# Performance work log

Hardware: AMD Instinct MI355X
Metric: run time of the kernel (lower is better)

Reference implementation:

```python
import jax, jax.numpy as jnp
import numpy as np

B, S, D, H = 4, 2048, 2048, 16
HD = D // H  # 128


def setup_inputs() -> dict:
    key = jax.random.key(0)
    k1, k2, k3 = jax.random.split(key, 3)
    sc = 1.0 / np.sqrt(D)
    return {
        "x": jax.random.normal(k1, (B, S, D), dtype=jnp.float32),
        "W_qkv": jax.random.normal(k2, (D, 3 * D), dtype=jnp.float32) * sc,
        "W_out": jax.random.normal(k3, (D, D), dtype=jnp.float32) * sc,
        "b_out": jnp.zeros((D,), dtype=jnp.float32),
    }


def _rotate_half(t):
    t1, t2 = jnp.split(t, 2, axis=-1)
    return jnp.concatenate([-t2, t1], axis=-1)


def reference(x, W_qkv, W_out, b_out):
    b, s, d = x.shape
    qkv = jnp.einsum('bsd,de->bse', x, W_qkv)  # fused QKV projection
    q, k, v = jnp.split(qkv, 3, axis=-1)
    # [b, h, s, hd]
    q = q.reshape(b, s, H, HD).transpose(0, 2, 1, 3)
    k = k.reshape(b, s, H, HD).transpose(0, 2, 1, 3)
    v = v.reshape(b, s, H, HD).transpose(0, 2, 1, 3)
    # RoPE (NeoX-style half-split), past_kv=None so positions = arange(s)
    pos = jnp.arange(s, dtype=jnp.float32)
    theta = 1.0 / (10000.0 ** (jnp.arange(0, HD, 2, dtype=jnp.float32) / HD))
    angles = pos[:, None] * theta[None, :]           # [s, hd/2]
    cos = jnp.concatenate([jnp.cos(angles)] * 2, -1)  # [s, hd] (repeat halves)
    sin = jnp.concatenate([jnp.sin(angles)] * 2, -1)
    cos = cos[None, None]  # [1,1,s,hd]
    sin = sin[None, None]
    q = q * cos + _rotate_half(q) * sin
    k = k * cos + _rotate_half(k) * sin
    # causal SDPA, scale = 1/sqrt(head_dim)
    scale = 1.0 / jnp.sqrt(jnp.asarray(HD, dtype=q.dtype))
    scores = jnp.einsum('bhqd,bhkd->bhqk', q, k) * scale
    causal = jnp.tril(jnp.ones((s, s), dtype=bool))
    scores = jnp.where(causal[None, None], scores, jnp.finfo(scores.dtype).min)
    attn = jax.nn.softmax(scores, axis=-1)
    out = jnp.einsum('bhqk,bhkd->bhqd', attn, v)
    out = out.transpose(0, 2, 1, 3).reshape(b, s, D)
    return jnp.einsum('bsd,de->bse', out, W_out) + b_out
```

## Files before the change

### kernel.cpp

```cpp
#include <hip/hip_runtime.h>

typedef unsigned short ushort_t;
typedef unsigned int u32;
typedef __attribute__((ext_vector_type(8))) short bf16x8;
typedef __attribute__((ext_vector_type(4))) float f32x4;

#define B_ 4
#define S_ 2048
#define D_ 2048
#define H_ 16
#define HD_ 128

__device__ __forceinline__ ushort_t f2bf(float f) {
  u32 x = __builtin_bit_cast(u32, f);
  x += 0x7fffu + ((x >> 16) & 1u);
  return (ushort_t)(x >> 16);
}
__device__ __forceinline__ float bf2f(ushort_t u) {
  u32 x = ((u32)u) << 16;
  return __builtin_bit_cast(float, x);
}

struct __align__(8) us4 { ushort_t x, y, z, w; };

__global__ void k_cvt_bf16(const float* __restrict__ in, ushort_t* __restrict__ out, int n) {
  int i = (blockIdx.x * 256 + threadIdx.x) * 4;
  if (i >= n) return;
  float4 v = *(const float4*)(in + i);
  us4 o;
  o.x = f2bf(v.x); o.y = f2bf(v.y); o.z = f2bf(v.z); o.w = f2bf(v.w);
  *(us4*)(out + i) = o;
}

__global__ void k_transpose_bf16(const float* __restrict__ in, ushort_t* __restrict__ out,
                                 int R, int C) {
  __shared__ float ld[32][33];
  int c0 = blockIdx.x * 32, r0 = blockIdx.y * 32;
  int tc = threadIdx.x & 31, tr = threadIdx.x >> 5;
#pragma unroll
  for (int i = 0; i < 4; ++i) {
    int r = tr + i * 8;
    ld[r][tc] = in[(size_t)(r0 + r) * C + c0 + tc];
  }
  __syncthreads();
#pragma unroll
  for (int i = 0; i < 4; ++i) {
    int r = tr + i * 8;
    out[(size_t)(c0 + r) * R + r0 + tc] = f2bf(ld[tc][r]);
  }
}

__global__ void k_rope_tables(float* __restrict__ cost, float* __restrict__ sint) {
  int i = blockIdx.x * 256 + threadIdx.x;
  int s = i >> 6, j = i & 63;
  double th = pow(10000.0, -(double)j / 64.0);
  double a = (double)s * th;
  cost[i] = (float)cos(a);
  sint[i] = (float)sin(a);
}

template <int FINAL>
__global__ __launch_bounds__(256, 2) void k_gemm_bt(const ushort_t* __restrict__ A,
                                                    const ushort_t* __restrict__ Bt,
                                                    void* __restrict__ Cout,
                                                    const float* __restrict__ bias,
                                                    int M, int N, int K) {
  __shared__ __attribute__((aligned(16))) ushort_t As[128 * 32];
  __shared__ __attribute__((aligned(16))) ushort_t Bs[128 * 32];
  const int tid = threadIdx.x;
  const int w = tid >> 6, l = tid & 63;
  const int lr = l & 15, lg = l >> 4;
  const int m0 = blockIdx.y * 128, n0 = blockIdx.x * 128;
  const int wr = (w >> 1) * 64, wc = (w & 1) * 64;
  f32x4 acc[4][4] = {};
  for (int kt = 0; kt < K; kt += 32) {
#pragma unroll
    for (int i = 0; i < 2; ++i) {
      int c = i * 256 + w * 64 + l;
      const ushort_t* ga = A + (size_t)(m0 + (c >> 2)) * K + kt + (c & 3) * 8;
      const ushort_t* gb = Bt + (size_t)(n0 + (c >> 2)) * K + kt + (c & 3) * 8;
      __builtin_amdgcn_global_load_lds(
          (const __attribute__((address_space(1))) u32*)ga,
          (__attribute__((address_space(3))) u32*)(As + (size_t)(i * 256 + w * 64) * 8), 16, 0, 0);
      __builtin_amdgcn_global_load_lds(
          (const __attribute__((address_space(1))) u32*)gb,
          (__attribute__((address_space(3))) u32*)(Bs + (size_t)(i * 256 + w * 64) * 8), 16, 0, 0);
    }
    __syncthreads();
    bf16x8 af[4], bfr[4];
#pragma unroll
    for (int m = 0; m < 4; ++m)
      af[m] = *(const bf16x8*)(As + (wr + m * 16 + lr) * 32 + lg * 8);
#pragma unroll
    for (int n = 0; n < 4; ++n)
      bfr[n] = *(const bf16x8*)(Bs + (wc + n * 16 + lr) * 32 + lg * 8);
#pragma unroll
    for (int m = 0; m < 4; ++m)
#pragma unroll
      for (int n = 0; n < 4; ++n)
        acc[m][n] = __builtin_amdgcn_mfma_f32_16x16x32_bf16(af[m], bfr[n], acc[m][n], 0, 0, 0);
    __syncthreads();
  }
#pragma unroll
  for (int m = 0; m < 4; ++m) {
#pragma unroll
    for (int n = 0; n < 4; ++n) {
#pragma unroll
      for (int j = 0; j < 4; ++j) {
        int row = m0 + wr + m * 16 + lg * 4 + j;
        int col = n0 + wc + n * 16 + lr;
        if (FINAL) {
          ((float*)Cout)[(size_t)row * N + col] = acc[m][n][j] + bias[col];
        } else {
          ((ushort_t*)Cout)[(size_t)row * N + col] = f2bf(acc[m][n][j]);
        }
      }
    }
  }
}

__global__ void k_split_rope(const ushort_t* __restrict__ tmp, ushort_t* __restrict__ dst,
                             const float* __restrict__ cost, const float* __restrict__ sint,
                             int mode) {
  int s0 = blockIdx.x * 32;
  int h = blockIdx.y;
  int b = blockIdx.z;
  int bh = b * H_ + h;
  if (mode < 2) {
#pragma unroll
    for (int i = 0; i < 16; ++i) {
      int e = i * 256 + threadIdx.x;
      int sr = e >> 7, d = e & 127;
      int s = s0 + sr;
      size_t base = (size_t)(b * S_ + s) * D_ + h * HD_;
      float v = bf2f(tmp[base + d]);
      int j = d & 63;
      float cth = cost[s * 64 + j], sth = sint[s * 64 + j];
      int pd = (d < 64) ? d + 64 : d - 64;
      float v2 = bf2f(tmp[base + pd]);
      float r = (d < 64) ? v * cth - v2 * sth : v * cth + v2 * sth;
      dst[((size_t)bh * S_ + s) * HD_ + d] = f2bf(r);
    }
  } else {
    __shared__ ushort_t ld[32][132];
#pragma unroll
    for (int i = 0; i < 16; ++i) {
      int e = i * 256 + threadIdx.x;
      int sr = e >> 7, d = e & 127;
      ld[sr][d] = tmp[(size_t)(b * S_ + s0 + sr) * D_ + h * HD_ + d];
    }
    __syncthreads();
#pragma unroll
    for (int i = 0; i < 16; ++i) {
      int e = i * 256 + threadIdx.x;
      int d = e >> 5, sr = e & 31;
      dst[((size_t)bh * HD_ + d) * S_ + s0 + sr] = ld[sr][d];
    }
  }
}

__global__ __launch_bounds__(256, 2) void k_attn2(const ushort_t* __restrict__ Q,
                                                  const ushort_t* __restrict__ K,
                                                  const ushort_t* __restrict__ Vt,
                                                  ushort_t* __restrict__ O) {
  __shared__ __attribute__((aligned(16))) ushort_t Ks[64 * 128];
  __shared__ __attribute__((aligned(16))) ushort_t Vs[128 * 64];
  __shared__ __attribute__((aligned(16))) ushort_t Pl[8][16 * 72];

  int id = blockIdx.x;
  int work = (id & 7) * 128 + (id >> 3);
  int bh = work >> 4;
  int qt = 15 - (work & 15);
  int b = bh >> 4, h = bh & 15;

  const int tid = threadIdx.x;
  const int w = tid >> 6, l = tid & 63;
  const int lr = l & 15, lg = l >> 4;
  const int qb = qt * 128 + w * 32;

  const ushort_t* Qp = Q + (size_t)bh * S_ * HD_;
  const char* Kpb = (const char*)(K + (size_t)bh * S_ * HD_);
  const char* Vpb = (const char*)(Vt + (size_t)bh * HD_ * S_);
  const float scale = 0.08838834764831845f;

  int krow[4], koff[4], vrow[4], voff[4];
#pragma unroll
  for (int r = 0; r < 4; ++r) {
    int c = r * 256 + tid;
    krow[r] = c >> 4;
    koff[r] = (((c & 15) ^ (krow[r] & 7)) << 4);
    vrow[r] = c >> 3;
    voff[r] = (((c & 7) ^ (vrow[r] & 7)) << 4);
  }
  const int swz = (lr & 7) << 4;

  bf16x8 qf[2][4];
#pragma unroll
  for (int f = 0; f < 2; ++f)
#pragma unroll
    for (int dw = 0; dw < 4; ++dw)
      qf[f][dw] = *(const bf16x8*)(Qp + (size_t)(qb + f * 16 + lr) * HD_ + dw * 32 + lg * 8);

  f32x4 oacc[2][8] = {};
  float mr[2] = {-1e30f, -1e30f};
  float lsum[2] = {0.f, 0.f};
  const int nkt = 2 * qt + 2;

  for (int kt = 0; kt < nkt; ++kt) {
    const int kb = kt * 64;
#pragma unroll
    for (int r = 0; r < 4; ++r) {
      __builtin_amdgcn_global_load_lds(
          (const __attribute__((address_space(1))) u32*)(Kpb + (size_t)(kb + krow[r]) * 256 + koff[r]),
          (__attribute__((address_space(3))) u32*)(Ks + (r * 256 + w * 64) * 8), 16, 0, 0);
    }
#pragma unroll
    for (int r = 0; r < 4; ++r) {
      __builtin_amdgcn_global_load_lds(
          (const __attribute__((address_space(1))) u32*)(Vpb + (size_t)vrow[r] * (S_ * 2) + kb * 2 + voff[r]),
          (__attribute__((address_space(3))) u32*)(Vs + (r * 256 + w * 64) * 8), 16, 0, 0);
    }
    __syncthreads();

    if (kb <= qb + 31) {
      f32x4 st[2][4];
      __builtin_amdgcn_s_setprio(1);
#pragma unroll
      for (int t = 0; t < 4; ++t) {
        bf16x8 kf[4];
#pragma unroll
        for (int dw = 0; dw < 4; ++dw)
          kf[dw] = *(const bf16x8*)((const char*)Ks + (t * 16 + lr) * 256 + ((dw * 64 + lg * 16) ^ swz));
        f32x4 a0 = {}, a1 = {};
#pragma unroll
        for (int dw = 0; dw < 4; ++dw) {
          a0 = __builtin_amdgcn_mfma_f32_16x16x32_bf16(kf[dw], qf[0][dw], a0, 0, 0, 0);
          a1 = __builtin_amdgcn_mfma_f32_16x16x32_bf16(kf[dw], qf[1][dw], a1, 0, 0, 0);
        }
        st[0][t] = a0;
        st[1][t] = a1;
      }
      __builtin_amdgcn_s_setprio(0);

#pragma unroll
      for (int f = 0; f < 2; ++f) {
        const int qg = qb + f * 16 + lr;
        float tmax = -1e30f;
#pragma unroll
        for (int t = 0; t < 4; ++t) {
#pragma unroll
          for (int j = 0; j < 4; ++j) {
            int kg = kb + t * 16 + lg * 4 + j;
            float s = st[f][t][j] * scale;
            s = (kg > qg) ? -1e30f : s;
            st[f][t][j] = s;
            tmax = fmaxf(tmax, s);
          }
        }
        tmax = fmaxf(tmax, __shfl_xor(tmax, 16, 64));
        tmax = fmaxf(tmax, __shfl_xor(tmax, 32, 64));
        float mnew = fmaxf(mr[f], tmax);
        float alpha = __expf(mr[f] - mnew);
        mr[f] = mnew;
        float psum = 0.f;
        ushort_t* Pw = Pl[w * 2 + f];
#pragma unroll
        for (int t = 0; t < 4; ++t) {
          float p0 = __expf(st[f][t][0] - mnew);
          float p1 = __expf(st[f][t][1] - mnew);
          float p2 = __expf(st[f][t][2] - mnew);
          float p3 = __expf(st[f][t][3] - mnew);
          psum += (p0 + p1) + (p2 + p3);
          *(u32*)&Pw[lr * 72 + t * 16 + lg * 4] = (u32)f2bf(p0) | ((u32)f2bf(p1) << 16);
          *(u32*)&Pw[lr * 72 + t * 16 + lg * 4 + 2] = (u32)f2bf(p2) | ((u32)f2bf(p3) << 16);
        }
        psum += __shfl_xor(psum, 16, 64);
        psum += __shfl_xor(psum, 32, 64);
        lsum[f] = lsum[f] * alpha + psum;
        float a0 = __shfl(alpha, lg * 4 + 0, 64);
        float a1 = __shfl(alpha, lg * 4 + 1, 64);
        float a2 = __shfl(alpha, lg * 4 + 2, 64);
        float a3 = __shfl(alpha, lg * 4 + 3, 64);
#pragma unroll
        for (int dt = 0; dt < 8; ++dt) {
          oacc[f][dt][0] *= a0;
          oacc[f][dt][1] *= a1;
          oacc[f][dt][2] *= a2;
          oacc[f][dt][3] *= a3;
        }
      }

      __builtin_amdgcn_s_setprio(1);
#pragma unroll
      for (int kw = 0; kw < 2; ++kw) {
        bf16x8 pa0 = *(const bf16x8*)&Pl[w * 2 + 0][lr * 72 + kw * 32 + lg * 8];
        bf16x8 pa1 = *(const bf16x8*)&Pl[w * 2 + 1][lr * 72 + kw * 32 + lg * 8];
#pragma unroll
        for (int dt = 0; dt < 8; ++dt) {
          bf16x8 vf = *(const bf16x8*)((const char*)Vs + (dt * 16 + lr) * 128 + ((kw * 64 + lg * 16) ^ swz));
          oacc[0][dt] = __builtin_amdgcn_mfma_f32_16x16x32_bf16(pa0, vf, oacc[0][dt], 0, 0, 0);
          oacc[1][dt] = __builtin_amdgcn_mfma_f32_16x16x32_bf16(pa1, vf, oacc[1][dt], 0, 0, 0);
        }
      }
      __builtin_amdgcn_s_setprio(0);
    }
    __syncthreads();
  }

#pragma unroll
  for (int f = 0; f < 2; ++f) {
    float l0 = __shfl(lsum[f], lg * 4 + 0, 64);
    float l1 = __shfl(lsum[f], lg * 4 + 1, 64);
    float l2 = __shfl(lsum[f], lg * 4 + 2, 64);
    float l3 = __shfl(lsum[f], lg * 4 + 3, 64);
    float i0 = 1.f / l0, i1 = 1.f / l1, i2 = 1.f / l2, i3 = 1.f / l3;
    ushort_t* Op = O + (size_t)(b * S_ + qb + f * 16) * D_ + h * HD_;
#pragma unroll
    for (int dt = 0; dt < 8; ++dt) {
      Op[(size_t)(lg * 4 + 0) * D_ + dt * 16 + lr] = f2bf(oacc[f][dt][0] * i0);
      Op[(size_t)(lg * 4 + 1) * D_ + dt * 16 + lr] = f2bf(oacc[f][dt][1] * i1);
      Op[(size_t)(lg * 4 + 2) * D_ + dt * 16 + lr] = f2bf(oacc[f][dt][2] * i2);
      Op[(size_t)(lg * 4 + 3) * D_ + dt * 16 + lr] = f2bf(oacc[f][dt][3] * i3);
    }
  }
}

extern "C" void kernel_launch(void* const* d_in, const int* in_sizes, int n_in,
                              void* d_out, int out_size, void* d_ws, size_t ws_size,
                              hipStream_t stream) {
  const float* x = (const float*)d_in[0];
  const float* Wqkv = (const float*)d_in[1];
  const float* Wout = (const float*)d_in[2];
  const float* bout = (const float*)d_in[3];
  char* ws = (char*)d_ws;

  ushort_t* xb = (ushort_t*)(ws + 0);
  ushort_t* Wqt = (ushort_t*)(ws + 33554432ull);
  ushort_t* tmp = (ushort_t*)(ws + 58720256ull);
  ushort_t* Qb = (ushort_t*)(ws + 92274688ull);
  ushort_t* Kb = (ushort_t*)(ws + 125829120ull);
  ushort_t* Vb = (ushort_t*)(ws + 159383552ull);
  float* cost = (float*)(ws + 192937984ull);
  float* sint = (float*)(ws + 193462272ull);

  const int M = B_ * S_;

  k_cvt_bf16<<<dim3((M * D_) / 4 / 256), 256, 0, stream>>>(x, xb, M * D_);
  k_transpose_bf16<<<dim3(3 * D_ / 32, D_ / 32), 256, 0, stream>>>(Wqkv, Wqt, D_, 3 * D_);
  k_rope_tables<<<dim3(S_ * 64 / 256), 256, 0, stream>>>(cost, sint);

  for (int p = 0; p < 3; ++p) {
    k_gemm_bt<0><<<dim3(D_ / 128, M / 128), 256, 0, stream>>>(
        xb, Wqt + (size_t)p * D_ * D_, tmp, nullptr, M, D_, D_);
    ushort_t* dst = (p == 0) ? Qb : (p == 1) ? Kb : Vb;
    k_split_rope<<<dim3(S_ / 32, H_, B_), 256, 0, stream>>>(tmp, dst, cost, sint, p);
  }

  k_attn2<<<dim3((S_ / 128) * B_ * H_), 256, 0, stream>>>(Qb, Kb, Vb, xb );

  k_transpose_bf16<<<dim3(D_ / 32, D_ / 32), 256, 0, stream>>>(Wout, tmp, D_, D_);
  k_gemm_bt<1><<<dim3(D_ / 128, M / 128), 256, 0, stream>>>(
      xb, tmp, d_out, bout, M, D_, D_);
}
```

Before: 590.6 us.

## Rewrite GEMM and attention with larger tiles and multi-buffered async loads

```diff
diff --git a/kernel.cpp b/kernel.cpp
--- a/kernel.cpp
+++ b/kernel.cpp
@@ -20,6 +20,11 @@
   u32 x = ((u32)u) << 16;
   return __builtin_bit_cast(float, x);
 }
+
+#define GLL16(srcp, ldsp)                                            \
+  __builtin_amdgcn_global_load_lds(                                  \
+      (const __attribute__((address_space(1))) u32*)(srcp),          \
+      (__attribute__((address_space(3))) u32*)(ldsp), 16, 0, 0)
 
 struct __align__(8) us4 { ushort_t x, y, z, w; };
 
@@ -60,63 +65,126 @@
 }
 
 template <int FINAL>
-__global__ __launch_bounds__(256, 2) void k_gemm_bt(const ushort_t* __restrict__ A,
+__global__ __launch_bounds__(512, 2) void k_gemm256(const ushort_t* __restrict__ A,
                                                     const ushort_t* __restrict__ Bt,
                                                     void* __restrict__ Cout,
                                                     const float* __restrict__ bias,
                                                     int M, int N, int K) {
-  __shared__ __attribute__((aligned(16))) ushort_t As[128 * 32];
-  __shared__ __attribute__((aligned(16))) ushort_t Bs[128 * 32];
+  __shared__ __attribute__((aligned(16))) ushort_t As[3][256 * 32];
+  __shared__ __attribute__((aligned(16))) ushort_t Bs[3][256 * 32];
   const int tid = threadIdx.x;
   const int w = tid >> 6, l = tid & 63;
   const int lr = l & 15, lg = l >> 4;
-  const int m0 = blockIdx.y * 128, n0 = blockIdx.x * 128;
-  const int wr = (w >> 1) * 64, wc = (w & 1) * 64;
-  f32x4 acc[4][4] = {};
-  for (int kt = 0; kt < K; kt += 32) {
-#pragma unroll
-    for (int i = 0; i < 2; ++i) {
-      int c = i * 256 + w * 64 + l;
-      const ushort_t* ga = A + (size_t)(m0 + (c >> 2)) * K + kt + (c & 3) * 8;
-      const ushort_t* gb = Bt + (size_t)(n0 + (c >> 2)) * K + kt + (c & 3) * 8;
-      __builtin_amdgcn_global_load_lds(
-          (const __attribute__((address_space(1))) u32*)ga,
-          (__attribute__((address_space(3))) u32*)(As + (size_t)(i * 256 + w * 64) * 8), 16, 0, 0);
-      __builtin_amdgcn_global_load_lds(
-          (const __attribute__((address_space(1))) u32*)gb,
-          (__attribute__((address_space(3))) u32*)(Bs + (size_t)(i * 256 + w * 64) * 8), 16, 0, 0);
-    }
-    __syncthreads();
-    bf16x8 af[4], bfr[4];
+  const int wrr = w >> 2, wcc = w & 3;
+
+  const int nbn = N >> 8;
+  const int cpx = gridDim.x >> 3;
+  const int bid = blockIdx.x;
+  const int swzid = (bid & 7) * cpx + (bid >> 3);
+  const size_t m0 = (size_t)(swzid / nbn) * 256;
+  const size_t n0 = (size_t)(swzid % nbn) * 256;
+
+  const size_t Kp = (size_t)K * 2;
+  const char* Ab = (const char*)A + (m0) * Kp;
+  const char* Bb = (const char*)Bt + (n0) * Kp;
+
+  const int row0 = tid >> 2, slot0 = tid & 3;
+  const int row1 = row0 + 128;
+  const int xa0 = ((slot0 ^ ((row0 >> 1) & 3)) << 4);
+  const int xa1 = ((slot0 ^ ((row1 >> 1) & 3)) << 4);
+
+#define STAGE_A(t, bb)                                                    \
+  {                                                                       \
+    GLL16(Ab + (size_t)row0 * Kp + (size_t)(t) * 64 + xa0,                \
+          (char*)As[bb] + (size_t)tid * 16);                              \
+    GLL16(Ab + (size_t)row1 * Kp + (size_t)(t) * 64 + xa1,                \
+          (char*)As[bb] + (size_t)(tid + 512) * 16);                      \
+  }
+#define STAGE_B(t, bb)                                                    \
+  {                                                                       \
+    GLL16(Bb + (size_t)row0 * Kp + (size_t)(t) * 64 + xa0,                \
+          (char*)Bs[bb] + (size_t)tid * 16);                              \
+    GLL16(Bb + (size_t)row1 * Kp + (size_t)(t) * 64 + xa1,                \
+          (char*)Bs[bb] + (size_t)(tid + 512) * 16);                      \
+  }
+
+  const int swz2 = (lr >> 1) & 3;
+  int aoff[8], boff[4];
+#pragma unroll
+  for (int m = 0; m < 8; ++m)
+    aoff[m] = (wrr * 128 + m * 16 + lr) * 64 + ((lg ^ swz2) << 4);
+#pragma unroll
+  for (int n = 0; n < 4; ++n)
+    boff[n] = (wcc * 64 + n * 16 + lr) * 64 + ((lg ^ swz2) << 4);
+
+  f32x4 acc[8][4] = {};
+  const int NT = K >> 5;
+
+  STAGE_A(0, 0); STAGE_B(0, 0);
+  STAGE_A(1, 1); STAGE_B(1, 1);
+  asm volatile("s_waitcnt vmcnt(4)");
+  __builtin_amdgcn_sched_barrier(0);
+  __builtin_amdgcn_s_barrier();
+
+  int bi = 0;
+  for (int t = 0; t < NT; ++t) {
+    int b2 = bi + 2; if (b2 >= 3) b2 -= 3;
+    const char* Ac = (const char*)As[bi];
+    const char* Bc = (const char*)Bs[bi];
+    if (t + 2 < NT) STAGE_A(t + 2, b2);
+    bf16x8 af0[4], bfr[4];
+#pragma unroll
+    for (int m = 0; m < 4; ++m) af0[m] = *(const bf16x8*)(Ac + aoff[m]);
+#pragma unroll
+    for (int n = 0; n < 4; ++n) bfr[n] = *(const bf16x8*)(Bc + boff[n]);
+    asm volatile("s_waitcnt lgkmcnt(0)");
+    __builtin_amdgcn_sched_barrier(0);
+    __builtin_amdgcn_s_setprio(1);
 #pragma unroll
     for (int m = 0; m < 4; ++m)
-      af[m] = *(const bf16x8*)(As + (wr + m * 16 + lr) * 32 + lg * 8);
-#pragma unroll
-    for (int n = 0; n < 4; ++n)
-      bfr[n] = *(const bf16x8*)(Bs + (wc + n * 16 + lr) * 32 + lg * 8);
+#pragma unroll
+      for (int n = 0; n < 4; ++n)
+        acc[m][n] = __builtin_amdgcn_mfma_f32_16x16x32_bf16(af0[m], bfr[n], acc[m][n], 0, 0, 0);
+    __builtin_amdgcn_s_setprio(0);
+    __builtin_amdgcn_s_barrier();
+    if (t + 2 < NT) STAGE_B(t + 2, b2);
+    bf16x8 af1[4];
+#pragma unroll
+    for (int m = 0; m < 4; ++m) af1[m] = *(const bf16x8*)(Ac + aoff[m + 4]);
+    asm volatile("s_waitcnt lgkmcnt(0)");
+    __builtin_amdgcn_sched_barrier(0);
+    __builtin_amdgcn_s_setprio(1);
 #pragma unroll
     for (int m = 0; m < 4; ++m)
 #pragma unroll
       for (int n = 0; n < 4; ++n)
-        acc[m][n] = __builtin_amdgcn_mfma_f32_16x16x32_bf16(af[m], bfr[n], acc[m][n], 0, 0, 0);
-    __syncthreads();
-  }
-#pragma unroll
-  for (int m = 0; m < 4; ++m) {
-#pragma unroll
-    for (int n = 0; n < 4; ++n) {
+        acc[m + 4][n] = __builtin_amdgcn_mfma_f32_16x16x32_bf16(af1[m], bfr[n], acc[m + 4][n], 0, 0, 0);
+    __builtin_amdgcn_s_setprio(0);
+    if (t + 1 < NT) {
+      if (t + 2 < NT) asm volatile("s_waitcnt vmcnt(4)");
+      else            asm volatile("s_waitcnt vmcnt(0)");
+      __builtin_amdgcn_sched_barrier(0);
+    }
+    __builtin_amdgcn_s_barrier();
+    bi = bi + 1; if (bi >= 3) bi = 0;
+  }
+
+#pragma unroll
+  for (int n = 0; n < 4; ++n) {
+    const size_t col = n0 + wcc * 64 + n * 16 + lr;
+    float bia = FINAL ? bias[col] : 0.f;
+#pragma unroll
+    for (int m = 0; m < 8; ++m) {
 #pragma unroll
       for (int j = 0; j < 4; ++j) {
-        int row = m0 + wr + m * 16 + lg * 4 + j;
-        int col = n0 + wc + n * 16 + lr;
-        if (FINAL) {
-          ((float*)Cout)[(size_t)row * N + col] = acc[m][n][j] + bias[col];
-        } else {
-          ((ushort_t*)Cout)[(size_t)row * N + col] = f2bf(acc[m][n][j]);
-        }
+        const size_t row = m0 + wrr * 128 + m * 16 + lg * 4 + j;
+        if (FINAL) ((float*)Cout)[row * N + col] = acc[m][n][j] + bia;
+        else       ((ushort_t*)Cout)[row * N + col] = f2bf(acc[m][n][j]);
       }
     }
   }
+#undef STAGE_A
+#undef STAGE_B
 }
 
 __global__ void k_split_rope(const ushort_t* __restrict__ tmp, ushort_t* __restrict__ dst,
@@ -159,40 +227,45 @@
   }
 }
 
-__global__ __launch_bounds__(256, 2) void k_attn2(const ushort_t* __restrict__ Q,
+__global__ __launch_bounds__(512, 2) void k_attn3(const ushort_t* __restrict__ Q,
                                                   const ushort_t* __restrict__ K,
                                                   const ushort_t* __restrict__ Vt,
                                                   ushort_t* __restrict__ O) {
-  __shared__ __attribute__((aligned(16))) ushort_t Ks[64 * 128];
-  __shared__ __attribute__((aligned(16))) ushort_t Vs[128 * 64];
-  __shared__ __attribute__((aligned(16))) ushort_t Pl[8][16 * 72];
-
-  int id = blockIdx.x;
-  int work = (id & 7) * 128 + (id >> 3);
-  int bh = work >> 4;
-  int qt = 15 - (work & 15);
-  int b = bh >> 4, h = bh & 15;
+  __shared__ __attribute__((aligned(16))) ushort_t Ks[2][64 * 128];
+  __shared__ __attribute__((aligned(16))) ushort_t Vs[2][128 * 64];
+  __shared__ __attribute__((aligned(16))) ushort_t Pl[16][16 * 72];
+
+  const int id = blockIdx.x;
+  const int work = (id & 7) * 64 + (id >> 3);
+  const int bh = work >> 3;
+  const int qt = 7 - (work & 7);
+  const int b = bh >> 4, h = bh & 15;
 
   const int tid = threadIdx.x;
   const int w = tid >> 6, l = tid & 63;
   const int lr = l & 15, lg = l >> 4;
-  const int qb = qt * 128 + w * 32;
+  const int qb = qt * 256 + w * 32;
 
   const ushort_t* Qp = Q + (size_t)bh * S_ * HD_;
   const char* Kpb = (const char*)(K + (size_t)bh * S_ * HD_);
   const char* Vpb = (const char*)(Vt + (size_t)bh * HD_ * S_);
-  const float scale = 0.08838834764831845f;
-
-  int krow[4], koff[4], vrow[4], voff[4];
-#pragma unroll
-  for (int r = 0; r < 4; ++r) {
-    int c = r * 256 + tid;
-    krow[r] = c >> 4;
-    koff[r] = (((c & 15) ^ (krow[r] & 7)) << 4);
-    vrow[r] = c >> 3;
-    voff[r] = (((c & 7) ^ (vrow[r] & 7)) << 4);
-  }
-  const int swz = (lr & 7) << 4;
+  const float kSc = 0.08838834764831845f * 1.4426950408889634f;
+
+  const int c1 = tid + 512;
+  const int kr0 = tid >> 4, ks0 = (((tid & 15) ^ (kr0 & 15)) << 4);
+  const int kr1 = c1 >> 4,  ks1 = (((c1 & 15) ^ (kr1 & 15)) << 4);
+  const int vr0 = tid >> 3, vs0 = (((tid & 7) ^ (vr0 & 7)) << 4);
+  const int vr1 = c1 >> 3,  vs1 = (((c1 & 7) ^ (vr1 & 7)) << 4);
+
+#define STAGE_KV(bufi, kb_)                                                     \
+  {                                                                             \
+    GLL16(Kpb + (size_t)((kb_) + kr0) * 256 + ks0, (char*)Ks[bufi] + (size_t)tid * 16); \
+    GLL16(Kpb + (size_t)((kb_) + kr1) * 256 + ks1, (char*)Ks[bufi] + (size_t)c1 * 16);  \
+    GLL16(Vpb + (size_t)vr0 * (S_ * 2) + (size_t)(kb_) * 2 + vs0,               \
+          (char*)Vs[bufi] + (size_t)tid * 16);                                  \
+    GLL16(Vpb + (size_t)vr1 * (S_ * 2) + (size_t)(kb_) * 2 + vs1,               \
+          (char*)Vs[bufi] + (size_t)c1 * 16);                                   \
+  }
 
   bf16x8 qf[2][4];
 #pragma unroll
@@ -204,25 +277,24 @@
   f32x4 oacc[2][8] = {};
   float mr[2] = {-1e30f, -1e30f};
   float lsum[2] = {0.f, 0.f};
-  const int nkt = 2 * qt + 2;
-
+  const int nkt = 4 * qt + 4;
+
+  STAGE_KV(0, 0);
   for (int kt = 0; kt < nkt; ++kt) {
     const int kb = kt * 64;
-#pragma unroll
-    for (int r = 0; r < 4; ++r) {
-      __builtin_amdgcn_global_load_lds(
-          (const __attribute__((address_space(1))) u32*)(Kpb + (size_t)(kb + krow[r]) * 256 + koff[r]),
-          (__attribute__((address_space(3))) u32*)(Ks + (r * 256 + w * 64) * 8), 16, 0, 0);
-    }
-#pragma unroll
-    for (int r = 0; r < 4; ++r) {
-      __builtin_amdgcn_global_load_lds(
-          (const __attribute__((address_space(1))) u32*)(Vpb + (size_t)vrow[r] * (S_ * 2) + kb * 2 + voff[r]),
-          (__attribute__((address_space(3))) u32*)(Vs + (r * 256 + w * 64) * 8), 16, 0, 0);
-    }
-    __syncthreads();
+    const int cur = kt & 1;
+    if (kt + 1 < nkt) {
+      STAGE_KV(cur ^ 1, kb + 64);
+      asm volatile("s_waitcnt vmcnt(4)");
+    } else {
+      asm volatile("s_waitcnt vmcnt(0)");
+    }
+    __builtin_amdgcn_sched_barrier(0);
+    __builtin_amdgcn_s_barrier();
 
     if (kb <= qb + 31) {
+      const char* Kc = (const char*)Ks[cur];
+      const char* Vc = (const char*)Vs[cur];
       f32x4 st[2][4];
       __builtin_amdgcn_s_setprio(1);
 #pragma unroll
@@ -230,7 +302,7 @@
         bf16x8 kf[4];
 #pragma unroll
         for (int dw = 0; dw < 4; ++dw)
-          kf[dw] = *(const bf16x8*)((const char*)Ks + (t * 16 + lr) * 256 + ((dw * 64 + lg * 16) ^ swz));
+          kf[dw] = *(const bf16x8*)(Kc + (t * 16 + lr) * 256 + (((dw * 4 + lg) ^ lr) << 4));
         f32x4 a0 = {}, a1 = {};
 #pragma unroll
         for (int dw = 0; dw < 4; ++dw) {
@@ -251,7 +323,7 @@
 #pragma unroll
           for (int j = 0; j < 4; ++j) {
             int kg = kb + t * 16 + lg * 4 + j;
-            float s = st[f][t][j] * scale;
+            float s = st[f][t][j] * kSc;
             s = (kg > qg) ? -1e30f : s;
             st[f][t][j] = s;
             tmax = fmaxf(tmax, s);
@@ -259,35 +331,38 @@
         }
         tmax = fmaxf(tmax, __shfl_xor(tmax, 16, 64));
         tmax = fmaxf(tmax, __shfl_xor(tmax, 32, 64));
-        float mnew = fmaxf(mr[f], tmax);
-        float alpha = __expf(mr[f] - mnew);
-        mr[f] = mnew;
+        if (!__all(tmax <= mr[f] + 8.f)) {
+          float mnew = fmaxf(mr[f], tmax);
+          float alpha = exp2f(mr[f] - mnew);
+          mr[f] = mnew;
+          lsum[f] *= alpha;
+          float a0 = __shfl(alpha, lg * 4 + 0, 64);
+          float a1 = __shfl(alpha, lg * 4 + 1, 64);
+          float a2 = __shfl(alpha, lg * 4 + 2, 64);
+          float a3 = __shfl(alpha, lg * 4 + 3, 64);
+#pragma unroll
+          for (int dt = 0; dt < 8; ++dt) {
+            oacc[f][dt][0] *= a0;
+            oacc[f][dt][1] *= a1;
+            oacc[f][dt][2] *= a2;
+            oacc[f][dt][3] *= a3;
+          }
+        }
         float psum = 0.f;
-        ushort_t* Pw = Pl[w * 2 + f];
+        ushort_t* Pw = (ushort_t*)Pl[w * 2 + f];
 #pragma unroll
         for (int t = 0; t < 4; ++t) {
-          float p0 = __expf(st[f][t][0] - mnew);
-          float p1 = __expf(st[f][t][1] - mnew);
-          float p2 = __expf(st[f][t][2] - mnew);
-          float p3 = __expf(st[f][t][3] - mnew);
+          float p0 = exp2f(st[f][t][0] - mr[f]);
+          float p1 = exp2f(st[f][t][1] - mr[f]);
+          float p2 = exp2f(st[f][t][2] - mr[f]);
+          float p3 = exp2f(st[f][t][3] - mr[f]);
           psum += (p0 + p1) + (p2 + p3);
           *(u32*)&Pw[lr * 72 + t * 16 + lg * 4] = (u32)f2bf(p0) | ((u32)f2bf(p1) << 16);
           *(u32*)&Pw[lr * 72 + t * 16 + lg * 4 + 2] = (u32)f2bf(p2) | ((u32)f2bf(p3) << 16);
         }
         psum += __shfl_xor(psum, 16, 64);
         psum += __shfl_xor(psum, 32, 64);
-        lsum[f] = lsum[f] * alpha + psum;
-        float a0 = __shfl(alpha, lg * 4 + 0, 64);
-        float a1 = __shfl(alpha, lg * 4 + 1, 64);
-        float a2 = __shfl(alpha, lg * 4 + 2, 64);
-        float a3 = __shfl(alpha, lg * 4 + 3, 64);
-#pragma unroll
-        for (int dt = 0; dt < 8; ++dt) {
-          oacc[f][dt][0] *= a0;
-          oacc[f][dt][1] *= a1;
-          oacc[f][dt][2] *= a2;
-          oacc[f][dt][3] *= a3;
-        }
+        lsum[f] += psum;
       }
 
       __builtin_amdgcn_s_setprio(1);
@@ -297,14 +372,14 @@
         bf16x8 pa1 = *(const bf16x8*)&Pl[w * 2 + 1][lr * 72 + kw * 32 + lg * 8];
 #pragma unroll
         for (int dt = 0; dt < 8; ++dt) {
-          bf16x8 vf = *(const bf16x8*)((const char*)Vs + (dt * 16 + lr) * 128 + ((kw * 64 + lg * 16) ^ swz));
+          bf16x8 vf = *(const bf16x8*)(Vc + (dt * 16 + lr) * 128 + (((kw * 4 + lg) ^ (lr & 7)) << 4));
           oacc[0][dt] = __builtin_amdgcn_mfma_f32_16x16x32_bf16(pa0, vf, oacc[0][dt], 0, 0, 0);
           oacc[1][dt] = __builtin_amdgcn_mfma_f32_16x16x32_bf16(pa1, vf, oacc[1][dt], 0, 0, 0);
         }
       }
       __builtin_amdgcn_s_setprio(0);
     }
-    __syncthreads();
+    __builtin_amdgcn_s_barrier();
   }
 
 #pragma unroll
@@ -323,6 +398,7 @@
       Op[(size_t)(lg * 4 + 3) * D_ + dt * 16 + lr] = f2bf(oacc[f][dt][3] * i3);
     }
   }
+#undef STAGE_KV
 }
 
 extern "C" void kernel_launch(void* const* d_in, const int* in_sizes, int n_in,
@@ -350,15 +426,15 @@
   k_rope_tables<<<dim3(S_ * 64 / 256), 256, 0, stream>>>(cost, sint);
 
   for (int p = 0; p < 3; ++p) {
-    k_gemm_bt<0><<<dim3(D_ / 128, M / 128), 256, 0, stream>>>(
+    k_gemm256<0><<<dim3((M / 256) * (D_ / 256)), 512, 0, stream>>>(
         xb, Wqt + (size_t)p * D_ * D_, tmp, nullptr, M, D_, D_);
     ushort_t* dst = (p == 0) ? Qb : (p == 1) ? Kb : Vb;
     k_split_rope<<<dim3(S_ / 32, H_, B_), 256, 0, stream>>>(tmp, dst, cost, sint, p);
   }
 
-  k_attn2<<<dim3((S_ / 128) * B_ * H_), 256, 0, stream>>>(Qb, Kb, Vb, xb );
+  k_attn3<<<dim3((S_ / 256) * B_ * H_), 512, 0, stream>>>(Qb, Kb, Vb, xb );
 
   k_transpose_bf16<<<dim3(D_ / 32, D_ / 32), 256, 0, stream>>>(Wout, tmp, D_, D_);
-  k_gemm_bt<1><<<dim3(D_ / 128, M / 128), 256, 0, stream>>>(
+  k_gemm256<1><<<dim3((M / 256) * (D_ / 256)), 512, 0, stream>>>(
       xb, tmp, d_out, bout, M, D_, D_);
 }
```

New measurement: 634.4 us. 1.07x slower.
